# Kernel optimization log

Hardware: AMD Instinct MI355X
Metric: run time of the kernel (lower is better)

Reference implementation:

```python
import jax, jax.numpy as jnp
import numpy as np

F0, F1 = 10, 10  # num_neighbor_list fanouts
B = 4096         # sampled pos+neg edges


def setup_inputs() -> dict:
    key = jax.random.key(0)
    ks = jax.random.split(key, 24)
    def rn(k, shp, scale=0.05):
        return (jax.random.normal(k, shp, dtype=jnp.float32) * scale)
    inp = {
        "user_feat": rn(ks[0], (50000, 512), 1.0),
        "item_feat": rn(ks[1], (100000, 512), 1.0),
        "W_pu": rn(ks[2], (512, 256)), "b_pu": jnp.zeros((256,), jnp.float32),
        "W_pi": rn(ks[3], (512, 256)), "b_pi": jnp.zeros((256,), jnp.float32),
        "u_self0": rn(ks[4], (256, 256)), "u_agg0": rn(ks[5], (256, 256)),
        "u_self1": rn(ks[6], (256, 128)), "u_agg1": rn(ks[7], (256, 128)),
        "i_self0": rn(ks[8], (256, 256)), "i_agg0": rn(ks[9], (256, 256)),
        "i_self1": rn(ks[10], (256, 128)), "i_agg1": rn(ks[11], (256, 128)),
        "W_lin": rn(ks[12], (128, 1)), "b_lin": jnp.zeros((1,), jnp.float32),
        # precomputed multi-hop sampled node ids (alternating user/item spaces)
        "src_h0": jax.random.randint(ks[13], (B,), 0, 50000, dtype=jnp.int32),
        "src_h1": jax.random.randint(ks[14], (B * F0,), 0, 100000, dtype=jnp.int32),
        "src_h2": jax.random.randint(ks[15], (B * F0 * F1,), 0, 50000, dtype=jnp.int32),
        "dst_h0": jax.random.randint(ks[16], (B,), 0, 100000, dtype=jnp.int32),
        "dst_h1": jax.random.randint(ks[17], (B * F0,), 0, 50000, dtype=jnp.int32),
        "dst_h2": jax.random.randint(ks[18], (B * F0 * F1,), 0, 100000, dtype=jnp.int32),
    }
    return inp


def _sage(h0, h1, h2, Wself0, Wagg0, Wself1, Wagg1):
    # 2-layer GraphSAGE with mean aggregation over fixed fanouts.
    d = h0.shape[-1]
    # layer 0: update hop-0 and hop-1 representations
    n0 = h1.reshape(h0.shape[0], F0, d).mean(axis=1)          # [B, d]
    g0 = jax.nn.relu(h0 @ Wself0 + n0 @ Wagg0)                # [B, H0]
    n1 = h2.reshape(h1.shape[0], F1, d).mean(axis=1)          # [B*F0, d]
    g1 = jax.nn.relu(h1 @ Wself0 + n1 @ Wagg0)                # [B*F0, H0]
    # layer 1: final hop-0 representation (no activation on last layer)
    n = g1.reshape(g0.shape[0], F0, -1).mean(axis=1)          # [B, H0]
    return g0 @ Wself1 + n @ Wagg1                            # [B, H1]


def reference(user_feat, item_feat, W_pu, b_pu, W_pi, b_pi,
              u_self0, u_agg0, u_self1, u_agg1,
              i_self0, i_agg0, i_self1, i_agg1,
              W_lin, b_lin,
              src_h0, src_h1, src_h2, dst_h0, dst_h1, dst_h2):
    u_proj = jax.nn.sigmoid(user_feat @ W_pu + b_pu)   # [U, P]
    i_proj = jax.nn.sigmoid(item_feat @ W_pi + b_pi)   # [I, P]
    # src side alternates user/item per hop; dst side alternates item/user
    user_h = _sage(u_proj[src_h0], i_proj[src_h1], u_proj[src_h2],
                   u_self0, u_agg0, u_self1, u_agg1)
    item_h = _sage(i_proj[dst_h0], u_proj[dst_h1], i_proj[dst_h2],
                   i_self0, i_agg0, i_self1, i_agg1)
    logits = (user_h * item_h) @ W_lin + b_lin          # [B, 1]
    return logits
```

## Files before the change

kernel.cpp:

```cpp
#include <hip/hip_runtime.h>
#include <hip/hip_bf16.h>
#include <type_traits>

typedef __attribute__((ext_vector_type(8))) short short8;
typedef __attribute__((ext_vector_type(4))) float f32x4;
typedef unsigned short u16;
typedef unsigned int u32;

typedef const __attribute__((address_space(1))) u32* gp1_t;
typedef __attribute__((address_space(3))) u32* lp3_t;

__device__ __forceinline__ float bf2f(u16 u) {
    union { unsigned int i; float f; } x; x.i = ((unsigned int)u) << 16; return x.f;
}
__device__ __forceinline__ u16 f2bf(float f) {
    union { __hip_bfloat16 h; u16 u; } c; c.h = __float2bfloat16(f); return c.u;
}
__device__ __forceinline__ short8 cvt8(float4 v0, float4 v1) {
    union { u16 u[8]; short8 s; } p;
    p.u[0] = f2bf(v0.x); p.u[1] = f2bf(v0.y); p.u[2] = f2bf(v0.z); p.u[3] = f2bf(v0.w);
    p.u[4] = f2bf(v1.x); p.u[5] = f2bf(v1.y); p.u[6] = f2bf(v1.z); p.u[7] = f2bf(v1.w);
    return p.s;
}
__device__ __forceinline__ void gload_lds16(const void* g, void* l) {
    __builtin_amdgcn_global_load_lds((gp1_t)g, (lp3_t)l, 16, 0, 0);
}

struct TCJobs {
    const float* A[6];
    const float* Bm[6];
    u16* out[6];
    int N[6];
    int Ka[6];
};

__global__ void transcat6_k(TCJobs j) {
    int jid = blockIdx.y;
    int i = blockIdx.x * 256 + threadIdx.x;
    int N = j.N[jid];
    if (i >= N * 512) return;
    int n = i >> 9, k = i & 511, Ka = j.Ka[jid];
    float v = (k < Ka) ? j.A[jid][k * N + n] : j.Bm[jid][(k - Ka) * N + n];
    j.out[jid][i] = f2bf(v);
}

struct GJob {
    const void* A;
    const u16* WT;
    const float* bias;
    void* C;
    int M;
    int nct;
    int toff;
};
struct GJobs4 { GJob j[4]; };

template <int NJ, bool F32A, int ACT, bool OF32>
__global__ __launch_bounds__(256, 4) void gemm_k(GJobs4 js) {
    const int K = 512;
    __shared__ __align__(1024) char As[F32A ? 16384 : 8192];
    __shared__ __align__(1024) char Bs[8192];
    const int t = threadIdx.x;
    const int lane = t & 63;
    const int wid = t >> 6;
    const int wr = wid >> 1, wc = wid & 1;
    const int lr = lane & 15;

    const int nwg = gridDim.x, p = blockIdx.x;
    const int q = nwg >> 3, rr = nwg & 7;
    const int xcd = p & 7, idx = p >> 3;
    const int L = (xcd < rr ? xcd * (q + 1) : rr * (q + 1) + (xcd - rr) * q) + idx;

    GJob jb = js.j[0];
    #pragma unroll
    for (int k = 1; k < NJ; ++k) if (L >= js.j[k].toff) jb = js.j[k];
    const int tl = L - jb.toff;
    const int rt = (jb.nct == 2) ? (tl >> 1) : tl;
    const int ct = (jb.nct == 2) ? (tl & 1) : 0;
    const int row_base = rt * 128, col_base = ct * 128;
    const int M = jb.M, N = jb.nct << 7;

    f32x4 acc[4][4] = {};

    for (int kt = 0; kt < K; kt += 32) {
        #pragma unroll
        for (int i = 0; i < 2; ++i) {
            int slot = wid * 2 + i;
            int rl = slot * 16 + (lane >> 2);
            int cc = lane & 3;
            gload_lds16(&jb.WT[(size_t)(col_base + rl) * K + kt + cc * 8], &Bs[slot * 1024]);
        }
        if constexpr (F32A) {
            #pragma unroll
            for (int i = 0; i < 4; ++i) {
                int slot = wid * 4 + i;
                int rl = slot * 8 + (lane >> 3);
                int sc = (lane & 7) ^ (rl & 7);
                int gr = row_base + rl; if (gr >= M) gr = M - 1;
                gload_lds16(&((const float*)jb.A)[(size_t)gr * K + kt + sc * 4],
                            &As[slot * 1024]);
            }
        } else {
            #pragma unroll
            for (int i = 0; i < 2; ++i) {
                int slot = wid * 2 + i;
                int rl = slot * 16 + (lane >> 2);
                int cc = lane & 3;
                int gr = row_base + rl; if (gr >= M) gr = M - 1;
                gload_lds16(&((const u16*)jb.A)[(size_t)gr * K + kt + cc * 8],
                            &As[slot * 1024]);
            }
        }
        __syncthreads();

        {
            const int g = lane >> 4;
            short8 a[4], b[4];
            #pragma unroll
            for (int ni = 0; ni < 4; ++ni) {
                int r = wc * 64 + ni * 16 + lr;
                b[ni] = *(const short8*)&Bs[r * 64 + g * 16];
            }
            #pragma unroll
            for (int mi = 0; mi < 4; ++mi) {
                int r = wr * 64 + mi * 16 + lr;
                if constexpr (F32A) {
                    float4 v0 = *(const float4*)&As[r * 128 + ((2 * g) ^ (r & 7)) * 16];
                    float4 v1 = *(const float4*)&As[r * 128 + ((2 * g + 1) ^ (r & 7)) * 16];
                    a[mi] = cvt8(v0, v1);
                } else {
                    a[mi] = *(const short8*)&As[r * 64 + g * 16];
                }
            }
            #pragma unroll
            for (int mi = 0; mi < 4; ++mi)
                #pragma unroll
                for (int ni = 0; ni < 4; ++ni)
                    acc[mi][ni] = __builtin_amdgcn_mfma_f32_16x16x32_bf16(
                        a[mi], b[ni], acc[mi][ni], 0, 0, 0);
        }
        __syncthreads();
    }

    #pragma unroll
    for (int mi = 0; mi < 4; ++mi) {
        int row0 = row_base + wr * 64 + mi * 16 + ((lane >> 4) << 2);
        #pragma unroll
        for (int ni = 0; ni < 4; ++ni) {
            int col = col_base + wc * 64 + ni * 16 + lr;
            float bv = jb.bias ? jb.bias[col] : 0.f;
            #pragma unroll
            for (int r = 0; r < 4; ++r) {
                int row = row0 + r;
                if (row < M) {
                    float x = acc[mi][ni][r] + bv;
                    if (ACT == 1) x = fmaxf(x, 0.f);
                    if (ACT == 2) x = 1.f / (1.f + __expf(-x));
                    if constexpr (OF32)
                        ((float*)jb.C)[(size_t)row * N + col] = x;
                    else
                        ((u16*)jb.C)[(size_t)row * N + col] = f2bf(x);
                }
            }
        }
    }
}

struct BJob {
    u16* X;
    const u16* selfP;
    const int* sidx;
    const u16* nbP;
    const int* nidx;
    int roff;
};
struct BJobs4 { BJob j[4]; };

template <int NJ>
__global__ void build_xm_k(BJobs4 bj, int total) {
    int gw = (int)((blockIdx.x * blockDim.x + threadIdx.x) >> 5);
    int hl = threadIdx.x & 31;
    if (gw >= total) return;
    BJob jb = bj.j[0];
    #pragma unroll
    for (int k = 1; k < NJ; ++k) if (gw >= bj.j[k].roff) jb = bj.j[k];
    int r = gw - jb.roff;

    int c8 = hl * 8;
    int sr = jb.sidx ? jb.sidx[r] : r;
    short8 sv = *(const short8*)&jb.selfP[(size_t)sr * 256 + c8];
    *(short8*)&jb.X[(size_t)r * 512 + c8] = sv;

    float s[8] = {};
    #pragma unroll
    for (int f = 0; f < 10; ++f) {
        int nr = jb.nidx ? jb.nidx[r * 10 + f] : r * 10 + f;
        short8 nv = *(const short8*)&jb.nbP[(size_t)nr * 256 + c8];
        #pragma unroll
        for (int jj = 0; jj < 8; ++jj) s[jj] += bf2f((u16)nv[jj]);
    }
    union { u16 u[8]; short8 v; } o;
    #pragma unroll
    for (int jj = 0; jj < 8; ++jj) o.u[jj] = f2bf(s[jj] * 0.1f);
    *(short8*)&jb.X[(size_t)r * 512 + 256 + c8] = o.v;
}

__global__ void logits_k(const float* __restrict__ hu, const float* __restrict__ hi,
                         const float* __restrict__ wlin, const float* __restrict__ blin,
                         float* __restrict__ out, int Bn) {
    int w = (blockIdx.x * blockDim.x + threadIdx.x) >> 6;
    int lane = threadIdx.x & 63;
    if (w >= Bn) return;
    float s = 0.f;
    #pragma unroll
    for (int k = lane; k < 128; k += 64)
        s += hu[(size_t)w * 128 + k] * hi[(size_t)w * 128 + k] * wlin[k];
    #pragma unroll
    for (int off = 32; off > 0; off >>= 1) s += __shfl_down(s, off, 64);
    if (lane == 0) out[w] = s + blin[0];
}

extern "C" void kernel_launch(void* const* d_in, const int* in_sizes, int n_in,
                              void* d_out, int out_size, void* d_ws, size_t ws_size,
                              hipStream_t stream) {
    const float* user_feat = (const float*)d_in[0];
    const float* item_feat = (const float*)d_in[1];
    const float* W_pu = (const float*)d_in[2];
    const float* b_pu = (const float*)d_in[3];
    const float* W_pi = (const float*)d_in[4];
    const float* b_pi = (const float*)d_in[5];
    const float* u_self0 = (const float*)d_in[6];
    const float* u_agg0 = (const float*)d_in[7];
    const float* u_self1 = (const float*)d_in[8];
    const float* u_agg1 = (const float*)d_in[9];
    const float* i_self0 = (const float*)d_in[10];
    const float* i_agg0 = (const float*)d_in[11];
    const float* i_self1 = (const float*)d_in[12];
    const float* i_agg1 = (const float*)d_in[13];
    const float* W_lin = (const float*)d_in[14];
    const float* b_lin = (const float*)d_in[15];
    const int* src_h0 = (const int*)d_in[16];
    const int* src_h1 = (const int*)d_in[17];
    const int* src_h2 = (const int*)d_in[18];
    const int* dst_h0 = (const int*)d_in[19];
    const int* dst_h1 = (const int*)d_in[20];
    const int* dst_h2 = (const int*)d_in[21];
    float* out = (float*)d_out;

    const int NU = 50000, NI = 100000, B = 4096, BF = 40960;

    char* ws = (char*)d_ws;
    size_t off = 0;
    auto alloc = [&](size_t bytes) -> void* {
        void* p = ws + off;
        off += (bytes + 255) & ~(size_t)255;
        return p;
    };
    u16* Pu   = (u16*)alloc((size_t)NU * 256 * 2);
    u16* Pi   = (u16*)alloc((size_t)NI * 256 * 2);
    u16* X1a  = (u16*)alloc((size_t)BF * 512 * 2);
    u16* X1b  = (u16*)alloc((size_t)BF * 512 * 2);
    u16* G1a  = (u16*)alloc((size_t)BF * 256 * 2);
    u16* G1b  = (u16*)alloc((size_t)BF * 256 * 2);
    u16* X0a  = (u16*)alloc((size_t)B * 512 * 2);
    u16* X0b  = (u16*)alloc((size_t)B * 512 * 2);
    u16* G0a  = (u16*)alloc((size_t)B * 256 * 2);
    u16* G0b  = (u16*)alloc((size_t)B * 256 * 2);
    u16* X2a  = (u16*)alloc((size_t)B * 512 * 2);
    u16* X2b  = (u16*)alloc((size_t)B * 512 * 2);
    float* Hu = (float*)alloc((size_t)B * 128 * 4);
    float* Hi = (float*)alloc((size_t)B * 128 * 4);
    u16* WpuT = (u16*)alloc(256 * 512 * 2);
    u16* WpiT = (u16*)alloc(256 * 512 * 2);
    u16* W0uT = (u16*)alloc(256 * 512 * 2);
    u16* W0iT = (u16*)alloc(256 * 512 * 2);
    u16* W1uT = (u16*)alloc(128 * 512 * 2);
    u16* W1iT = (u16*)alloc(128 * 512 * 2);

    TCJobs tj;
    tj.A[0] = W_pu;    tj.Bm[0] = W_pu;    tj.out[0] = WpuT; tj.N[0] = 256; tj.Ka[0] = 512;
    tj.A[1] = W_pi;    tj.Bm[1] = W_pi;    tj.out[1] = WpiT; tj.N[1] = 256; tj.Ka[1] = 512;
    tj.A[2] = u_self0; tj.Bm[2] = u_agg0;  tj.out[2] = W0uT; tj.N[2] = 256; tj.Ka[2] = 256;
    tj.A[3] = i_self0; tj.Bm[3] = i_agg0;  tj.out[3] = W0iT; tj.N[3] = 256; tj.Ka[3] = 256;
    tj.A[4] = u_self1; tj.Bm[4] = u_agg1;  tj.out[4] = W1uT; tj.N[4] = 128; tj.Ka[4] = 256;
    tj.A[5] = i_self1; tj.Bm[5] = i_agg1;  tj.out[5] = W1iT; tj.N[5] = 128; tj.Ka[5] = 256;
    transcat6_k<<<dim3(512, 6), 256, 0, stream>>>(tj);

    const int ptu = ((NU + 127) / 128) * 2;
    const int pti = ((NI + 127) / 128) * 2;
    GJobs4 pj;
    pj.j[0] = {user_feat, WpuT, b_pu, Pu, NU, 2, 0};
    pj.j[1] = {item_feat, WpiT, b_pi, Pi, NI, 2, ptu};
    pj.j[2] = pj.j[1]; pj.j[3] = pj.j[1];
    gemm_k<2, true, 2, false><<<ptu + pti, 256, 0, stream>>>(pj);

    BJobs4 b1;
    b1.j[0] = {X1a, Pi, src_h1, Pu, src_h2, 0};
    b1.j[1] = {X1b, Pu, dst_h1, Pi, dst_h2, BF};
    b1.j[2] = {X0a, Pu, src_h0, Pi, src_h1, 2 * BF};
    b1.j[3] = {X0b, Pi, dst_h0, Pu, dst_h1, 2 * BF + B};
    const int tot1 = 2 * BF + 2 * B;
    build_xm_k<4><<<tot1 / 8, 256, 0, stream>>>(b1, tot1);

    GJobs4 sj;
    sj.j[0] = {X1a, W0uT, nullptr, G1a, BF, 2, 0};
    sj.j[1] = {X1b, W0iT, nullptr, G1b, BF, 2, 640};
    sj.j[2] = {X0a, W0uT, nullptr, G0a, B, 2, 1280};
    sj.j[3] = {X0b, W0iT, nullptr, G0b, B, 2, 1344};
    gemm_k<4, false, 1, false><<<1408, 256, 0, stream>>>(sj);

    BJobs4 b2;
    b2.j[0] = {X2a, G0a, nullptr, G1a, nullptr, 0};
    b2.j[1] = {X2b, G0b, nullptr, G1b, nullptr, B};
    b2.j[2] = b2.j[1]; b2.j[3] = b2.j[1];
    build_xm_k<2><<<(2 * B) / 8, 256, 0, stream>>>(b2, 2 * B);

    GJobs4 fj;
    fj.j[0] = {X2a, W1uT, nullptr, Hu, B, 1, 0};
    fj.j[1] = {X2b, W1iT, nullptr, Hi, B, 1, 32};
    fj.j[2] = fj.j[1]; fj.j[3] = fj.j[1];
    gemm_k<2, false, 0, true><<<64, 256, 0, stream>>>(fj);

    logits_k<<<B / 4, 256, 0, stream>>>(Hu, Hi, W_lin, b_lin, out, B);
}
```

Measured before the change: 307.0 us.

## Triple-buffer GEMM LDS tiles with async prefetch and XOR-swizzled bf16 layout

Restructures the GEMM main loop into a three-stage software pipeline. Global-to-LDS loads for tile k+2 are issued before computing tile k, with explicit vmcnt waits and barriers replacing the two __syncthreads per iteration. Also XOR-swizzles the bf16 A and B LDS layouts to reduce bank conflicts on the short8 reads. LDS use triples, so launch bounds drop to 2 blocks per CU, trading occupancy for overlap of memory latency.

```diff
diff --git a/kernel.cpp b/kernel.cpp
--- a/kernel.cpp
+++ b/kernel.cpp
@@ -9,6 +9,10 @@
 
 typedef const __attribute__((address_space(1))) u32* gp1_t;
 typedef __attribute__((address_space(3))) u32* lp3_t;
+
+#define VMW(n) asm volatile("s_waitcnt vmcnt(" #n ")" ::: "memory")
+#define SCHB() __builtin_amdgcn_sched_barrier(0)
+#define SBAR() __builtin_amdgcn_s_barrier()
 
 __device__ __forceinline__ float bf2f(u16 u) {
     union { unsigned int i; float f; } x; x.i = ((unsigned int)u) << 16; return x.f;
@@ -56,10 +60,11 @@
 struct GJobs4 { GJob j[4]; };
 
 template <int NJ, bool F32A, int ACT, bool OF32>
-__global__ __launch_bounds__(256, 4) void gemm_k(GJobs4 js) {
+__global__ __launch_bounds__(256, 2) void gemm_k(GJobs4 js) {
     const int K = 512;
-    __shared__ __align__(1024) char As[F32A ? 16384 : 8192];
-    __shared__ __align__(1024) char Bs[8192];
+    constexpr int ASZ = F32A ? 16384 : 8192;
+    __shared__ __align__(1024) char As[3 * ASZ];
+    __shared__ __align__(1024) char Bs[3 * 8192];
     const int t = threadIdx.x;
     const int lane = t & 63;
     const int wid = t >> 6;
@@ -82,14 +87,17 @@
 
     f32x4 acc[4][4] = {};
 
-    for (int kt = 0; kt < K; kt += 32) {
+    auto stage = [&](int kt, int pb) {
+        char* bs = &Bs[pb * 8192];
         #pragma unroll
         for (int i = 0; i < 2; ++i) {
             int slot = wid * 2 + i;
             int rl = slot * 16 + (lane >> 2);
-            int cc = lane & 3;
-            gload_lds16(&jb.WT[(size_t)(col_base + rl) * K + kt + cc * 8], &Bs[slot * 1024]);
-        }
+            int cc = (lane & 3) ^ (rl & 3);
+            gload_lds16(&jb.WT[(size_t)(col_base + rl) * K + kt + cc * 8],
+                        &bs[slot * 1024]);
+        }
+        char* as = &As[pb * ASZ];
         if constexpr (F32A) {
             #pragma unroll
             for (int i = 0; i < 4; ++i) {
@@ -98,49 +106,71 @@
                 int sc = (lane & 7) ^ (rl & 7);
                 int gr = row_base + rl; if (gr >= M) gr = M - 1;
                 gload_lds16(&((const float*)jb.A)[(size_t)gr * K + kt + sc * 4],
-                            &As[slot * 1024]);
+                            &as[slot * 1024]);
             }
         } else {
             #pragma unroll
             for (int i = 0; i < 2; ++i) {
                 int slot = wid * 2 + i;
                 int rl = slot * 16 + (lane >> 2);
-                int cc = lane & 3;
+                int cc = (lane & 3) ^ (rl & 3);
                 int gr = row_base + rl; if (gr >= M) gr = M - 1;
                 gload_lds16(&((const u16*)jb.A)[(size_t)gr * K + kt + cc * 8],
-                            &As[slot * 1024]);
+                            &as[slot * 1024]);
             }
         }
-        __syncthreads();
-
-        {
-            const int g = lane >> 4;
-            short8 a[4], b[4];
+    };
+
+    auto compute = [&](int pb) {
+        const char* as = &As[pb * ASZ];
+        const char* bs = &Bs[pb * 8192];
+        const int g = lane >> 4;
+        short8 a[4], b[4];
+        #pragma unroll
+        for (int ni = 0; ni < 4; ++ni) {
+            int r = wc * 64 + ni * 16 + lr;
+            b[ni] = *(const short8*)&bs[r * 64 + ((g ^ (r & 3)) * 16)];
+        }
+        #pragma unroll
+        for (int mi = 0; mi < 4; ++mi) {
+            int r = wr * 64 + mi * 16 + lr;
+            if constexpr (F32A) {
+                float4 v0 = *(const float4*)&as[r * 128 + (((2 * g) ^ (r & 7)) * 16)];
+                float4 v1 = *(const float4*)&as[r * 128 + (((2 * g + 1) ^ (r & 7)) * 16)];
+                a[mi] = cvt8(v0, v1);
+            } else {
+                a[mi] = *(const short8*)&as[r * 64 + ((g ^ (r & 3)) * 16)];
+            }
+        }
+        #pragma unroll
+        for (int mi = 0; mi < 4; ++mi)
             #pragma unroll
-            for (int ni = 0; ni < 4; ++ni) {
-                int r = wc * 64 + ni * 16 + lr;
-                b[ni] = *(const short8*)&Bs[r * 64 + g * 16];
-            }
-            #pragma unroll
-            for (int mi = 0; mi < 4; ++mi) {
-                int r = wr * 64 + mi * 16 + lr;
-                if constexpr (F32A) {
-                    float4 v0 = *(const float4*)&As[r * 128 + ((2 * g) ^ (r & 7)) * 16];
-                    float4 v1 = *(const float4*)&As[r * 128 + ((2 * g + 1) ^ (r & 7)) * 16];
-                    a[mi] = cvt8(v0, v1);
-                } else {
-                    a[mi] = *(const short8*)&As[r * 64 + g * 16];
-                }
-            }
-            #pragma unroll
-            for (int mi = 0; mi < 4; ++mi)
-                #pragma unroll
-                for (int ni = 0; ni < 4; ++ni)
-                    acc[mi][ni] = __builtin_amdgcn_mfma_f32_16x16x32_bf16(
-                        a[mi], b[ni], acc[mi][ni], 0, 0, 0);
-        }
-        __syncthreads();
+            for (int ni = 0; ni < 4; ++ni)
+                acc[mi][ni] = __builtin_amdgcn_mfma_f32_16x16x32_bf16(
+                    a[mi], b[ni], acc[mi][ni], 0, 0, 0);
+    };
+
+    stage(0, 0);
+    stage(32, 1);
+    int pb2 = 2;
+    int pbc = 0;
+    for (int tt = 0; tt < 14; ++tt) {
+        stage((tt + 2) << 5, pb2);
+        if constexpr (F32A) VMW(12); else VMW(8);
+        SCHB(); SBAR(); SCHB();
+        compute(pbc);
+        SBAR();
+        pb2 = (pb2 == 2) ? 0 : pb2 + 1;
+        pbc = (pbc == 2) ? 0 : pbc + 1;
     }
+    if constexpr (F32A) VMW(6); else VMW(4);
+    SCHB(); SBAR(); SCHB();
+    compute(pbc);
+    SBAR();
+    pbc = (pbc == 2) ? 0 : pbc + 1;
+    VMW(0);
+    SCHB(); SBAR(); SCHB();
+    compute(pbc);
 
     #pragma unroll
     for (int mi = 0; mi < 4; ++mi) {
```

Measured after the change: 347.1 us. +13.1%, slower.

## Widen GEMM tiles to full output width and swizzle bf16 LDS layout

Applied to the files above, without the earlier changes.

The GEMM kernel is templated on the number of column waves, so the N=256 GEMMs now use 512-thread blocks whose 128x256 tile covers the full output width. Each A tile is therefore loaded once instead of twice across two column tiles, which halves reads of the large float32 feature matrices and the layer-0 inputs. An XOR swizzle is also added to the bf16 A and B LDS layouts to reduce bank conflicts on the MFMA operand reads. The cost is larger blocks with more LDS each, which may lower occupancy, and half as many workgroups per launch.

```diff
diff --git a/kernel.cpp b/kernel.cpp
--- a/kernel.cpp
+++ b/kernel.cpp
@@ -50,20 +50,20 @@
     const float* bias;
     void* C;
     int M;
-    int nct;
     int toff;
 };
 struct GJobs4 { GJob j[4]; };
 
-template <int NJ, bool F32A, int ACT, bool OF32>
-__global__ __launch_bounds__(256, 4) void gemm_k(GJobs4 js) {
+template <int NJ, int WC, bool F32A, int ACT, bool OF32>
+__global__ __launch_bounds__(WC * 128, 4) void gemm_k(GJobs4 js) {
     const int K = 512;
+    const int N = WC * 64;
     __shared__ __align__(1024) char As[F32A ? 16384 : 8192];
-    __shared__ __align__(1024) char Bs[8192];
+    __shared__ __align__(1024) char Bs[WC * 4096];
     const int t = threadIdx.x;
     const int lane = t & 63;
     const int wid = t >> 6;
-    const int wr = wid >> 1, wc = wid & 1;
+    const int wr = wid / WC, wc = wid % WC;
     const int lr = lane & 15;
 
     const int nwg = gridDim.x, p = blockIdx.x;
@@ -74,11 +74,8 @@
     GJob jb = js.j[0];
     #pragma unroll
     for (int k = 1; k < NJ; ++k) if (L >= js.j[k].toff) jb = js.j[k];
-    const int tl = L - jb.toff;
-    const int rt = (jb.nct == 2) ? (tl >> 1) : tl;
-    const int ct = (jb.nct == 2) ? (tl & 1) : 0;
-    const int row_base = rt * 128, col_base = ct * 128;
-    const int M = jb.M, N = jb.nct << 7;
+    const int row_base = (L - jb.toff) * 128;
+    const int M = jb.M;
 
     f32x4 acc[4][4] = {};
 
@@ -87,13 +84,13 @@
         for (int i = 0; i < 2; ++i) {
             int slot = wid * 2 + i;
             int rl = slot * 16 + (lane >> 2);
-            int cc = lane & 3;
-            gload_lds16(&jb.WT[(size_t)(col_base + rl) * K + kt + cc * 8], &Bs[slot * 1024]);
+            int cc = (lane & 3) ^ ((rl >> 1) & 3);
+            gload_lds16(&jb.WT[(size_t)rl * K + kt + cc * 8], &Bs[slot * 1024]);
         }
         if constexpr (F32A) {
             #pragma unroll
-            for (int i = 0; i < 4; ++i) {
-                int slot = wid * 4 + i;
+            for (int i = 0; i < 16 / (2 * WC); ++i) {
+                int slot = wid * (16 / (2 * WC)) + i;
                 int rl = slot * 8 + (lane >> 3);
                 int sc = (lane & 7) ^ (rl & 7);
                 int gr = row_base + rl; if (gr >= M) gr = M - 1;
@@ -102,10 +99,10 @@
             }
         } else {
             #pragma unroll
-            for (int i = 0; i < 2; ++i) {
-                int slot = wid * 2 + i;
+            for (int i = 0; i < 8 / (2 * WC); ++i) {
+                int slot = wid * (8 / (2 * WC)) + i;
                 int rl = slot * 16 + (lane >> 2);
-                int cc = lane & 3;
+                int cc = (lane & 3) ^ ((rl >> 1) & 3);
                 int gr = row_base + rl; if (gr >= M) gr = M - 1;
                 gload_lds16(&((const u16*)jb.A)[(size_t)gr * K + kt + cc * 8],
                             &As[slot * 1024]);
@@ -119,17 +116,17 @@
             #pragma unroll
             for (int ni = 0; ni < 4; ++ni) {
                 int r = wc * 64 + ni * 16 + lr;
-                b[ni] = *(const short8*)&Bs[r * 64 + g * 16];
+                b[ni] = *(const short8*)&Bs[r * 64 + ((g ^ ((r >> 1) & 3)) * 16)];
             }
             #pragma unroll
             for (int mi = 0; mi < 4; ++mi) {
                 int r = wr * 64 + mi * 16 + lr;
                 if constexpr (F32A) {
-                    float4 v0 = *(const float4*)&As[r * 128 + ((2 * g) ^ (r & 7)) * 16];
-                    float4 v1 = *(const float4*)&As[r * 128 + ((2 * g + 1) ^ (r & 7)) * 16];
+                    float4 v0 = *(const float4*)&As[r * 128 + (((2 * g) ^ (r & 7)) * 16)];
+                    float4 v1 = *(const float4*)&As[r * 128 + (((2 * g + 1) ^ (r & 7)) * 16)];
                     a[mi] = cvt8(v0, v1);
                 } else {
-                    a[mi] = *(const short8*)&As[r * 64 + g * 16];
+                    a[mi] = *(const short8*)&As[r * 64 + ((g ^ ((r >> 1) & 3)) * 16)];
                 }
             }
             #pragma unroll
@@ -147,7 +144,7 @@
         int row0 = row_base + wr * 64 + mi * 16 + ((lane >> 4) << 2);
         #pragma unroll
         for (int ni = 0; ni < 4; ++ni) {
-            int col = col_base + wc * 64 + ni * 16 + lr;
+            int col = wc * 64 + ni * 16 + lr;
             float bv = jb.bias ? jb.bias[col] : 0.f;
             #pragma unroll
             for (int r = 0; r < 4; ++r) {
@@ -286,13 +283,13 @@
     tj.A[5] = i_self1; tj.Bm[5] = i_agg1;  tj.out[5] = W1iT; tj.N[5] = 128; tj.Ka[5] = 256;
     transcat6_k<<<dim3(512, 6), 256, 0, stream>>>(tj);
 
-    const int ptu = ((NU + 127) / 128) * 2;
-    const int pti = ((NI + 127) / 128) * 2;
+    const int ptu = (NU + 127) / 128;
+    const int pti = (NI + 127) / 128;
     GJobs4 pj;
-    pj.j[0] = {user_feat, WpuT, b_pu, Pu, NU, 2, 0};
-    pj.j[1] = {item_feat, WpiT, b_pi, Pi, NI, 2, ptu};
+    pj.j[0] = {user_feat, WpuT, b_pu, Pu, NU, 0};
+    pj.j[1] = {item_feat, WpiT, b_pi, Pi, NI, ptu};
     pj.j[2] = pj.j[1]; pj.j[3] = pj.j[1];
-    gemm_k<2, true, 2, false><<<ptu + pti, 256, 0, stream>>>(pj);
+    gemm_k<2, 4, true, 2, false><<<ptu + pti, 512, 0, stream>>>(pj);
 
     BJobs4 b1;
     b1.j[0] = {X1a, Pi, src_h1, Pu, src_h2, 0};
@@ -303,11 +300,11 @@
     build_xm_k<4><<<tot1 / 8, 256, 0, stream>>>(b1, tot1);
 
     GJobs4 sj;
-    sj.j[0] = {X1a, W0uT, nullptr, G1a, BF, 2, 0};
-    sj.j[1] = {X1b, W0iT, nullptr, G1b, BF, 2, 640};
-    sj.j[2] = {X0a, W0uT, nullptr, G0a, B, 2, 1280};
-    sj.j[3] = {X0b, W0iT, nullptr, G0b, B, 2, 1344};
-    gemm_k<4, false, 1, false><<<1408, 256, 0, stream>>>(sj);
+    sj.j[0] = {X1a, W0uT, nullptr, G1a, BF, 0};
+    sj.j[1] = {X1b, W0iT, nullptr, G1b, BF, 320};
+    sj.j[2] = {X0a, W0uT, nullptr, G0a, B, 640};
+    sj.j[3] = {X0b, W0iT, nullptr, G0b, B, 672};
+    gemm_k<4, 4, false, 1, false><<<704, 512, 0, stream>>>(sj);
 
     BJobs4 b2;
     b2.j[0] = {X2a, G0a, nullptr, G1a, nullptr, 0};
@@ -316,10 +313,10 @@
     build_xm_k<2><<<(2 * B) / 8, 256, 0, stream>>>(b2, 2 * B);
 
     GJobs4 fj;
-    fj.j[0] = {X2a, W1uT, nullptr, Hu, B, 1, 0};
-    fj.j[1] = {X2b, W1iT, nullptr, Hi, B, 1, 32};
+    fj.j[0] = {X2a, W1uT, nullptr, Hu, B, 0};
+    fj.j[1] = {X2b, W1iT, nullptr, Hi, B, 32};
     fj.j[2] = fj.j[1]; fj.j[3] = fj.j[1];
-    gemm_k<2, false, 0, true><<<64, 256, 0, stream>>>(fj);
+    gemm_k<2, 2, false, 0, true><<<64, 256, 0, stream>>>(fj);
 
     logits_k<<<B / 4, 256, 0, stream>>>(Hu, Hi, W_lin, b_lin, out, B);
 }
```

New measurement: 304.6 us (median of 2 runs). About the same (-0.8%).
